# Performance work log

Hardware: AMD Instinct MI355X
Metric: run time of the kernel (lower is better)

The kernel has to match this reference:

```python
import jax, jax.numpy as jnp
import numpy as np

N_NODES = 20000
N_EDGES = 320000
NEG_SLOPE = 0.2


def gat_conv(x, src, dst, W, a_src, a_dst, b, concat):
    # x: [N, Fin]; W: [Fin, H*C]; a_src/a_dst: [H, C]; b: [H*C] or [C]
    N = x.shape[0]
    H, C = a_src.shape
    h = (x @ W).reshape(N, H, C)                      # [N, H, C]
    al_s = jnp.einsum('nhc,hc->nh', h, a_src)         # [N, H]
    al_d = jnp.einsum('nhc,hc->nh', h, a_dst)         # [N, H]
    e = jax.nn.leaky_relu(al_s[src] + al_d[dst], NEG_SLOPE)  # [E, H]
    # segment softmax over incoming edges of each dst node
    m = jax.ops.segment_max(e, dst, num_segments=N)   # [N, H]
    ex = jnp.exp(e - m[dst])
    denom = jax.ops.segment_sum(ex, dst, num_segments=N)
    alpha = ex / denom[dst]                           # [E, H]
    msg = alpha[:, :, None] * h[src]                  # [E, H, C]
    out = jax.ops.segment_sum(msg, dst, num_segments=N)  # [N, H, C]
    if concat:
        return out.reshape(N, H * C) + b
    return out.mean(axis=1) + b


def setup_inputs() -> dict:
    key = jax.random.key(0)
    ks = jax.random.split(key, 16)
    def g(k, shape, scale=0.05):
        return jax.random.normal(k, shape, dtype=jnp.float32) * scale
    x = jax.random.normal(ks[0], (N_NODES, 768), dtype=jnp.float32)
    edge_index = jax.random.randint(ks[1], (2, N_EDGES), 0, N_NODES, dtype=jnp.int32)
    return {
        'x': x, 'edge_index': edge_index,
        'W1': g(ks[2], (768, 1024)), 'a1_src': g(ks[3], (4, 256)), 'a1_dst': g(ks[4], (4, 256)), 'b1': g(ks[5], (1024,)),
        'W2': g(ks[6], (1024, 512)), 'a2_src': g(ks[7], (4, 128)), 'a2_dst': g(ks[8], (4, 128)), 'b2': g(ks[9], (512,)),
        'W3': g(ks[10], (512, 64)), 'a3_src': g(ks[11], (1, 64)), 'a3_dst': g(ks[12], (1, 64)), 'b3': g(ks[13], (64,)),
    }


def reference(x, edge_index, W1, a1_src, a1_dst, b1, W2, a2_src, a2_dst, b2, W3, a3_src, a3_dst, b3):
    N = x.shape[0]
    loops = jnp.arange(N, dtype=edge_index.dtype)
    src = jnp.concatenate([edge_index[0], loops])  # PyG GATConv adds self-loops
    dst = jnp.concatenate([edge_index[1], loops])
    h = gat_conv(x, src, dst, W1, a1_src, a1_dst, b1, concat=True)
    h = jax.nn.relu(h)
    h = gat_conv(h, src, dst, W2, a2_src, a2_dst, b2, concat=True)
    h = jax.nn.relu(h)
    h = gat_conv(h, src, dst, W3, a3_src, a3_dst, b3, concat=False)
    return jnp.tanh(h)
```

## Files before the change

kernel.cpp:

```cpp
#include <hip/hip_runtime.h>
#include <hip/hip_bf16.h>

#define NN 20000
#define NE 320000
#define ET 340000
#define NEG_SLOPE 0.2f

typedef __attribute__((ext_vector_type(8))) _Float16 f16x8;
typedef __attribute__((ext_vector_type(4))) _Float16 f16x4;
typedef __attribute__((ext_vector_type(4))) float f32x4;

typedef __attribute__((address_space(3))) unsigned int lds_u32_t;
typedef __attribute__((address_space(1))) unsigned int glb_u32_t;

__device__ __forceinline__ void gload_lds16(const void* g, void* l) {
  __builtin_amdgcn_global_load_lds((const glb_u32_t*)g, (lds_u32_t*)l, 16, 0, 0);
}

__global__ void k_zero(int* p, int n) {
  int i = blockIdx.x * blockDim.x + threadIdx.x;
  if (i < n) p[i] = 0;
}

__global__ void k_count(const int* __restrict__ ei, int* __restrict__ cnt) {
  int e = blockIdx.x * blockDim.x + threadIdx.x;
  if (e >= ET) return;
  int d = (e < NE) ? ei[NE + e] : (e - NE);
  atomicAdd(&cnt[d], 1);
}

__global__ __launch_bounds__(1024) void k_scan(const int* __restrict__ cnt,
                                               int* __restrict__ rptr,
                                               int* __restrict__ cursor) {
  const int CH = 20;
  int t = threadIdx.x, lane = t & 63, wid = t >> 6;
  int base = t * CH;
  int v[CH];
  int sum = 0;
#pragma unroll
  for (int j = 0; j < CH; ++j) {
    int idx = base + j;
    v[j] = (idx < NN) ? cnt[idx] : 0;
    sum += v[j];
  }
  int ws = sum;
#pragma unroll
  for (int off = 1; off < 64; off <<= 1) {
    int u = __shfl_up(ws, off);
    if (lane >= off) ws += u;
  }
  __shared__ int wsum[16];
  __shared__ int wpre[16];
  if (lane == 63) wsum[wid] = ws;
  __syncthreads();
  if (t == 0) {
    int acc = 0;
#pragma unroll
    for (int w = 0; w < 16; ++w) { wpre[w] = acc; acc += wsum[w]; }
  }
  __syncthreads();
  int run = wpre[wid] + ws - sum;
  if (t == 0) rptr[0] = 0;
#pragma unroll
  for (int j = 0; j < CH; ++j) {
    int idx = base + j;
    if (idx < NN) {
      cursor[idx] = run;
      run += v[j];
      rptr[idx + 1] = run;
    }
  }
}

__global__ void k_fill(const int* __restrict__ ei, int* __restrict__ cursor,
                       int* __restrict__ csrc) {
  int e = blockIdx.x * blockDim.x + threadIdx.x;
  if (e >= ET) return;
  int s, d;
  if (e < NE) { s = ei[e]; d = ei[NE + e]; } else { s = d = e - NE; }
  int p = atomicAdd(&cursor[d], 1);
  csrc[p] = s;
}

__global__ void k_f2h4(const float* __restrict__ x, _Float16* __restrict__ o, int n4) {
  int i = blockIdx.x * blockDim.x + threadIdx.x;
  if (i >= n4) return;
  f32x4 v = *(const f32x4*)&x[i * 4];
  f16x4 h = { (_Float16)v.x, (_Float16)v.y, (_Float16)v.z, (_Float16)v.w };
  *(f16x4*)&o[i * 4] = h;
}

__global__ __launch_bounds__(256) void k_wt(const float* __restrict__ W,
                                            _Float16* __restrict__ Wt, int K, int N) {
  __shared__ float tile[32][33];
  int bk = blockIdx.y * 32, bn = blockIdx.x * 32;
  int tx = threadIdx.x & 31, ty = threadIdx.x >> 5;
#pragma unroll
  for (int r = ty; r < 32; r += 8) {
    int k = bk + r, n = bn + tx;
    tile[r][tx] = (k < K && n < N) ? W[(size_t)k * N + n] : 0.f;
  }
  __syncthreads();
#pragma unroll
  for (int r = ty; r < 32; r += 8) {
    int n = bn + r, k = bk + tx;
    if (n < N && k < K) Wt[(size_t)n * K + k] = (_Float16)tile[tx][r];
  }
}

__global__ __launch_bounds__(256) void k_gemm(const _Float16* __restrict__ A,
                                              const _Float16* __restrict__ B,
                                              _Float16* __restrict__ C,
                                              const float* __restrict__ a_src,
                                              const float* __restrict__ a_dst,
                                              float* __restrict__ als,
                                              float* __restrict__ ald,
                                              int M, int N, int K, int gx,
                                              int H, int Ch) {
  const int nb = gridDim.x;
  const int q = nb >> 3, r = nb & 7;
  const int xcd = blockIdx.x & 7, kk = blockIdx.x >> 3;
  const int l = (xcd < r) ? (xcd * (q + 1) + kk) : (r * (q + 1) + (xcd - r) * q + kk);
  const int bx = l % gx, by = l / gx;

  __shared__ __align__(16) _Float16 Al[128 * 32];
  __shared__ __align__(16) _Float16 Bl[128 * 32];
  const int tid = threadIdx.x;
  const int wave = tid >> 6, lane = tid & 63;
  const int wm = wave >> 1, wn = wave & 1;
  const int m0 = by * 128, n0 = bx * 128;
  const int fr = lane & 15, fk = (lane >> 4) * 8;
  f32x4 acc[4][4] = {};

  for (int k0 = 0; k0 < K; k0 += 32) {
#pragma unroll
    for (int c = 0; c < 2; ++c) {
      int s = (wave * 2 + c) * 64 + lane;
      int row = s >> 2, col = (s & 3) * 8;
      int ra = m0 + row; if (ra > M - 1) ra = M - 1;
      int rb = n0 + row; if (rb > N - 1) rb = N - 1;
      gload_lds16(A + (size_t)ra * K + k0 + col, &Al[(size_t)(wave * 2 + c) * 512]);
      gload_lds16(B + (size_t)rb * K + k0 + col, &Bl[(size_t)(wave * 2 + c) * 512]);
    }
    __syncthreads();
    f16x8 af[4], bf[4];
#pragma unroll
    for (int i = 0; i < 4; ++i) {
      af[i] = *(const f16x8*)&Al[(wm * 64 + i * 16 + fr) * 32 + fk];
      bf[i] = *(const f16x8*)&Bl[(wn * 64 + i * 16 + fr) * 32 + fk];
    }
#pragma unroll
    for (int mi = 0; mi < 4; ++mi)
#pragma unroll
      for (int ni = 0; ni < 4; ++ni)
        acc[mi][ni] = __builtin_amdgcn_mfma_f32_16x16x32_f16(af[mi], bf[ni], acc[mi][ni], 0, 0, 0);
    __syncthreads();
  }

  const int r0 = (lane >> 4) * 4, cn = lane & 15;

#pragma unroll
  for (int mi = 0; mi < 4; ++mi)
#pragma unroll
    for (int ni = 0; ni < 4; ++ni) {
      int gm = m0 + wm * 64 + mi * 16 + r0;
      int gn = n0 + wn * 64 + ni * 16 + cn;
      if (gn < N) {
#pragma unroll
        for (int rr = 0; rr < 4; ++rr)
          if (gm + rr < M) C[(size_t)(gm + rr) * N + gn] = (_Float16)acc[mi][ni][rr];
      }
    }

  const int colbase = n0 + wn * 64;
  if (colbase < N) {
    const int hd = colbase / Ch;
    const int cin = colbase % Ch;
    float asv[4], adv[4];
#pragma unroll
    for (int ni = 0; ni < 4; ++ni) {
      int cc = colbase + ni * 16 + cn;
      bool ok = cc < N;
      int ci = hd * Ch + cin + ni * 16 + cn;
      asv[ni] = ok ? a_src[ci] : 0.f;
      adv[ni] = ok ? a_dst[ci] : 0.f;
    }
#pragma unroll
    for (int mi = 0; mi < 4; ++mi) {
#pragma unroll
      for (int rr = 0; rr < 4; ++rr) {
        float sv = 0.f, dv = 0.f;
#pragma unroll
        for (int ni = 0; ni < 4; ++ni) {
          sv += acc[mi][ni][rr] * asv[ni];
          dv += acc[mi][ni][rr] * adv[ni];
        }
#pragma unroll
        for (int off = 1; off < 16; off <<= 1) {
          sv += __shfl_xor(sv, off);
          dv += __shfl_xor(dv, off);
        }
        if ((lane & 15) == 0) {
          int gm = m0 + wm * 64 + mi * 16 + r0 + rr;
          if (gm < M) {
            atomicAdd(&als[gm * H + hd], sv);
            atomicAdd(&ald[gm * H + hd], dv);
          }
        }
      }
    }
  }
}

template <int H, int C, int MODE>
__global__ __launch_bounds__(256) void k_aggw(
    const _Float16* __restrict__ h, const float* __restrict__ als,
    const float* __restrict__ ald, const int* __restrict__ rptr,
    const int* __restrict__ csrc, const float* __restrict__ bias,
    _Float16* __restrict__ oh, float* __restrict__ of) {
  constexpr int HC = H * C;
  constexpr int CPL = HC / 64;
  constexpr int NV = CPL / 8;
  const int wave = threadIdx.x >> 6, lane = threadIdx.x & 63;
  const int n = blockIdx.x * 4 + wave;
  const int c0 = lane * CPL;
  const int hd = c0 / C;
  const float aldn = ald[n * H + hd];
  const int e0 = rptr[n], e1 = rptr[n + 1];
  float acc[CPL];
#pragma unroll
  for (int j = 0; j < CPL; ++j) acc[j] = 0.f;
  float den = 0.f;

  float lA = 0.f, lB = 0.f;
  f16x8 hA[NV], hB[NV];

#define LD_ROW(I, L, HV)                                                     \
  do {                                                                       \
    int _i = (I);                                                            \
    if (_i < e1) {                                                           \
      int _s = csrc[_i];                                                     \
      (L) = als[_s * H + hd];                                                \
      const _Float16* _hp = h + (size_t)_s * HC + c0;                        \
      _Pragma("unroll")                                                      \
      for (int _v = 0; _v < NV; ++_v) (HV)[_v] = *(const f16x8*)(_hp + _v * 8); \
    }                                                                        \
  } while (0)

  LD_ROW(e0, lA, hA);
  LD_ROW(e0 + 1, lB, hB);

  for (int i = e0; i < e1; i += 2) {
    {
      float v = lA + aldn;
      f16x8 t[NV];
#pragma unroll
      for (int vv = 0; vv < NV; ++vv) t[vv] = hA[vv];
      LD_ROW(i + 2, lA, hA);
      v = v > 0.f ? v : NEG_SLOPE * v;
      float xv = __expf(v);
      den += xv;
#pragma unroll
      for (int vv = 0; vv < NV; ++vv)
#pragma unroll
        for (int j = 0; j < 8; ++j) acc[vv * 8 + j] += xv * (float)t[vv][j];
    }
    if (i + 1 < e1) {
      float v = lB + aldn;
      f16x8 t[NV];
#pragma unroll
      for (int vv = 0; vv < NV; ++vv) t[vv] = hB[vv];
      LD_ROW(i + 3, lB, hB);
      v = v > 0.f ? v : NEG_SLOPE * v;
      float xv = __expf(v);
      den += xv;
#pragma unroll
      for (int vv = 0; vv < NV; ++vv)
#pragma unroll
        for (int j = 0; j < 8; ++j) acc[vv * 8 + j] += xv * (float)t[vv][j];
    }
  }
#undef LD_ROW

  float invd = 1.f / den;
#pragma unroll
  for (int v = 0; v < NV; ++v) {
    f16x8 o;
#pragma unroll
    for (int j = 0; j < 8; ++j) {
      float r = acc[v * 8 + j] * invd + bias[c0 + v * 8 + j];
      o[j] = (_Float16)(r > 0.f ? r : 0.f);
    }
    __builtin_nontemporal_store(o, (f16x8*)&oh[(size_t)n * HC + c0 + v * 8]);
  }
}

__global__ __launch_bounds__(64) void k_agg_last(
    const _Float16* __restrict__ h, const float* __restrict__ als,
    const float* __restrict__ ald, const int* __restrict__ rptr,
    const int* __restrict__ csrc, const float* __restrict__ bias,
    float* __restrict__ of) {
  int n = blockIdx.x;
  int t = threadIdx.x;
  float acc = 0.f, den = 0.f;
  float aldn = ald[n];
  int e0 = rptr[n], e1 = rptr[n + 1];
  for (int i = e0; i < e1; ++i) {
    int s = csrc[i];
    float v = als[s] + aldn;
    v = v > 0.f ? v : NEG_SLOPE * v;
    float xv = __expf(v);
    den += xv;
    acc += xv * (float)h[(size_t)s * 64 + t];
  }
  of[(size_t)n * 64 + t] = tanhf(acc / den + bias[t]);
}

static inline size_t alup(size_t x) { return (x + 255) & ~(size_t)255; }

struct Scratch {
  _Float16* xb; _Float16* wtb; _Float16* h;
  float* als; float* ald;
  int* cnt; int* rptr; int* cursor; int* csrc;
};

static void run_layer(hipStream_t stream, const Scratch& S, const _Float16* xin,
                      int K, int N, int H, int C,
                      const float* W, const float* as_, const float* ad_, const float* bias,
                      int mode, _Float16* oh, float* of) {
  dim3 gt((N + 31) / 32, (K + 31) / 32);
  k_wt<<<gt, 256, 0, stream>>>(W, S.wtb, K, N);
  k_zero<<<(2 * NN * H + 255) / 256, 256, 0, stream>>>((int*)S.als, 2 * NN * H);
  int gx = (N + 127) / 128, gy = (NN + 127) / 128;
  k_gemm<<<gx * gy, 256, 0, stream>>>(xin, S.wtb, S.h, as_, ad_, S.als, S.ald,
                                      NN, N, K, gx, H, C);
  if (mode == 0) {
    if (C == 256)      k_aggw<4, 256, 0><<<NN / 4, 256, 0, stream>>>(S.h, S.als, S.ald, S.rptr, S.csrc, bias, oh, of);
    else if (C == 128) k_aggw<4, 128, 0><<<NN / 4, 256, 0, stream>>>(S.h, S.als, S.ald, S.rptr, S.csrc, bias, oh, of);
  } else {
    k_agg_last<<<NN, 64, 0, stream>>>(S.h, S.als, S.ald, S.rptr, S.csrc, bias, of);
  }
}

extern "C" void kernel_launch(void* const* d_in, const int* in_sizes, int n_in,
                              void* d_out, int out_size, void* d_ws, size_t ws_size,
                              hipStream_t stream) {
  const float* x   = (const float*)d_in[0];
  const int*   ei  = (const int*)d_in[1];
  const float* W1  = (const float*)d_in[2];
  const float* a1s = (const float*)d_in[3];
  const float* a1d = (const float*)d_in[4];
  const float* b1  = (const float*)d_in[5];
  const float* W2  = (const float*)d_in[6];
  const float* a2s = (const float*)d_in[7];
  const float* a2d = (const float*)d_in[8];
  const float* b2  = (const float*)d_in[9];
  const float* W3  = (const float*)d_in[10];
  const float* a3s = (const float*)d_in[11];
  const float* a3d = (const float*)d_in[12];
  const float* b3  = (const float*)d_in[13];
  float* out = (float*)d_out;

  char* p = (char*)d_ws;
  Scratch S;
  S.xb  = (_Float16*)p; p += alup((size_t)NN * 1024 * 2);
  S.wtb = (_Float16*)p; p += alup((size_t)1024 * 1024 * 2);
  S.h   = (_Float16*)p; p += alup((size_t)NN * 1024 * 2);
  S.als = (float*)p;    p += alup((size_t)2 * NN * 4 * 4);
  S.ald = S.als + NN * 4;
  S.cnt = (int*)p;      p += alup((size_t)NN * 4);
  S.rptr= (int*)p;      p += alup((size_t)(NN + 1) * 4);
  S.cursor=(int*)p;     p += alup((size_t)NN * 4);
  S.csrc= (int*)p;      p += alup((size_t)ET * 4);


  k_zero<<<(NN + 255) / 256, 256, 0, stream>>>(S.cnt, NN);
  k_count<<<(ET + 255) / 256, 256, 0, stream>>>(ei, S.cnt);
  k_scan<<<1, 1024, 0, stream>>>(S.cnt, S.rptr, S.cursor);
  k_fill<<<(ET + 255) / 256, 256, 0, stream>>>(ei, S.cursor, S.csrc);

  k_f2h4<<<(NN * 768 / 4 + 255) / 256, 256, 0, stream>>>(x, S.xb, NN * 768 / 4);

  S.ald = S.als + NN * 4;
  run_layer(stream, S, S.xb, 768, 1024, 4, 256, W1, a1s, a1d, b1, 0, S.xb, nullptr);
  S.ald = S.als + NN * 4;
  run_layer(stream, S, S.xb, 1024, 512, 4, 128, W2, a2s, a2d, b2, 0, S.xb, nullptr);
  S.ald = S.als + NN * 1;
  run_layer(stream, S, S.xb, 512, 64, 1, 64, W3, a3s, a3d, b3, 1, nullptr, out);
}
```

Measured before the change: 441.1 us.

## Split GAT aggregation across eight feature slices per node group

Replaces the wave-per-node aggregation kernel with one that splits each node's feature vector into eight slices, each handled by a separate block. Each lane now accumulates one or two channels instead of up to sixteen, and the two-deep software prefetch of neighbour rows is removed. The aim is more concurrent waves and lower register pressure to hide gather latency. In exchange, the CSR index and attention-logit reads are repeated for every slice, and the per-lane loads become narrow 2- or 4-byte accesses.

```diff
diff --git a/kernel.cpp b/kernel.cpp
--- a/kernel.cpp
+++ b/kernel.cpp
@@ -8,6 +8,7 @@
 
 typedef __attribute__((ext_vector_type(8))) _Float16 f16x8;
 typedef __attribute__((ext_vector_type(4))) _Float16 f16x4;
+typedef __attribute__((ext_vector_type(2))) _Float16 f16x2;
 typedef __attribute__((ext_vector_type(4))) float f32x4;
 
 typedef __attribute__((address_space(3))) unsigned int lds_u32_t;
@@ -212,86 +213,50 @@
   }
 }
 
-template <int H, int C, int MODE>
-__global__ __launch_bounds__(256) void k_aggw(
+template <int H, int C>
+__global__ __launch_bounds__(256) void k_aggs(
     const _Float16* __restrict__ h, const float* __restrict__ als,
     const float* __restrict__ ald, const int* __restrict__ rptr,
     const int* __restrict__ csrc, const float* __restrict__ bias,
-    _Float16* __restrict__ oh, float* __restrict__ of) {
+    _Float16* __restrict__ oh) {
   constexpr int HC = H * C;
-  constexpr int CPL = HC / 64;
-  constexpr int NV = CPL / 8;
+  constexpr int SC = HC / 8;
+  constexpr int CPL = SC / 64;
+  const int sl = blockIdx.x & 7;
+  const int grp = blockIdx.x >> 3;
   const int wave = threadIdx.x >> 6, lane = threadIdx.x & 63;
-  const int n = blockIdx.x * 4 + wave;
-  const int c0 = lane * CPL;
-  const int hd = c0 / C;
+  const int n = grp * 4 + wave;
+  const int c0 = sl * SC + lane * CPL;
+  const int hd = (sl * SC) / C;
   const float aldn = ald[n * H + hd];
   const int e0 = rptr[n], e1 = rptr[n + 1];
-  float acc[CPL];
-#pragma unroll
-  for (int j = 0; j < CPL; ++j) acc[j] = 0.f;
-  float den = 0.f;
-
-  float lA = 0.f, lB = 0.f;
-  f16x8 hA[NV], hB[NV];
-
-#define LD_ROW(I, L, HV)                                                     \
-  do {                                                                       \
-    int _i = (I);                                                            \
-    if (_i < e1) {                                                           \
-      int _s = csrc[_i];                                                     \
-      (L) = als[_s * H + hd];                                                \
-      const _Float16* _hp = h + (size_t)_s * HC + c0;                        \
-      _Pragma("unroll")                                                      \
-      for (int _v = 0; _v < NV; ++_v) (HV)[_v] = *(const f16x8*)(_hp + _v * 8); \
-    }                                                                        \
-  } while (0)
-
-  LD_ROW(e0, lA, hA);
-  LD_ROW(e0 + 1, lB, hB);
-
-  for (int i = e0; i < e1; i += 2) {
-    {
-      float v = lA + aldn;
-      f16x8 t[NV];
-#pragma unroll
-      for (int vv = 0; vv < NV; ++vv) t[vv] = hA[vv];
-      LD_ROW(i + 2, lA, hA);
-      v = v > 0.f ? v : NEG_SLOPE * v;
-      float xv = __expf(v);
-      den += xv;
-#pragma unroll
-      for (int vv = 0; vv < NV; ++vv)
-#pragma unroll
-        for (int j = 0; j < 8; ++j) acc[vv * 8 + j] += xv * (float)t[vv][j];
-    }
-    if (i + 1 < e1) {
-      float v = lB + aldn;
-      f16x8 t[NV];
-#pragma unroll
-      for (int vv = 0; vv < NV; ++vv) t[vv] = hB[vv];
-      LD_ROW(i + 3, lB, hB);
-      v = v > 0.f ? v : NEG_SLOPE * v;
-      float xv = __expf(v);
-      den += xv;
-#pragma unroll
-      for (int vv = 0; vv < NV; ++vv)
-#pragma unroll
-        for (int j = 0; j < 8; ++j) acc[vv * 8 + j] += xv * (float)t[vv][j];
-    }
-  }
-#undef LD_ROW
+
+  float acc0 = 0.f, acc1 = 0.f, den = 0.f;
+  for (int i = e0; i < e1; ++i) {
+    int s = csrc[i];
+    float v = als[s * H + hd] + aldn;
+    v = v > 0.f ? v : NEG_SLOPE * v;
+    float xv = __expf(v);
+    den += xv;
+    if (CPL == 2) {
+      f16x2 hv = *(const f16x2*)&h[(size_t)s * HC + c0];
+      acc0 += xv * (float)hv[0];
+      acc1 += xv * (float)hv[1];
+    } else {
+      acc0 += xv * (float)h[(size_t)s * HC + c0];
+    }
+  }
 
   float invd = 1.f / den;
-#pragma unroll
-  for (int v = 0; v < NV; ++v) {
-    f16x8 o;
-#pragma unroll
-    for (int j = 0; j < 8; ++j) {
-      float r = acc[v * 8 + j] * invd + bias[c0 + v * 8 + j];
-      o[j] = (_Float16)(r > 0.f ? r : 0.f);
-    }
-    __builtin_nontemporal_store(o, (f16x8*)&oh[(size_t)n * HC + c0 + v * 8]);
+  if (CPL == 2) {
+    float r0 = acc0 * invd + bias[c0];
+    float r1 = acc1 * invd + bias[c0 + 1];
+    f16x2 o = { (_Float16)(r0 > 0.f ? r0 : 0.f), (_Float16)(r1 > 0.f ? r1 : 0.f) };
+    __builtin_nontemporal_store(o, (f16x2*)&oh[(size_t)n * HC + c0]);
+  } else {
+    float r0 = acc0 * invd + bias[c0];
+    __builtin_nontemporal_store((_Float16)(r0 > 0.f ? r0 : 0.f),
+                                &oh[(size_t)n * HC + c0]);
   }
 }
 
@@ -335,8 +300,8 @@
   k_gemm<<<gx * gy, 256, 0, stream>>>(xin, S.wtb, S.h, as_, ad_, S.als, S.ald,
                                       NN, N, K, gx, H, C);
   if (mode == 0) {
-    if (C == 256)      k_aggw<4, 256, 0><<<NN / 4, 256, 0, stream>>>(S.h, S.als, S.ald, S.rptr, S.csrc, bias, oh, of);
-    else if (C == 128) k_aggw<4, 128, 0><<<NN / 4, 256, 0, stream>>>(S.h, S.als, S.ald, S.rptr, S.csrc, bias, oh, of);
+    if (C == 256)      k_aggs<4, 256><<<8 * (NN / 4), 256, 0, stream>>>(S.h, S.als, S.ald, S.rptr, S.csrc, bias, oh);
+    else if (C == 128) k_aggs<4, 128><<<8 * (NN / 4), 256, 0, stream>>>(S.h, S.als, S.ald, S.rptr, S.csrc, bias, oh);
   } else {
     k_agg_last<<<NN, 64, 0, stream>>>(S.h, S.als, S.ald, S.rptr, S.csrc, bias, of);
   }
@@ -373,7 +338,6 @@
   S.cursor=(int*)p;     p += alup((size_t)NN * 4);
   S.csrc= (int*)p;      p += alup((size_t)ET * 4);
 
-
   k_zero<<<(NN + 255) / 256, 256, 0, stream>>>(S.cnt, NN);
   k_count<<<(ET + 255) / 256, 256, 0, stream>>>(ei, S.cnt);
   k_scan<<<1, 1024, 0, stream>>>(S.cnt, S.rptr, S.cursor);
```

Result: slower. 690.2 us (+56.5%).
